# Optimization experiments

Measured on AMD Instinct MI355X. Metric: run time of the kernel, lower is better.

The kernel has to match this reference:

```python
import jax, jax.numpy as jnp
import numpy as np

N_NODES = 100000
N_EDGES = 1600000
NFEAT = 512
NHID = 64
NCLASS = 40


def setup_inputs() -> dict:
    key = jax.random.key(0)
    ks = jax.random.split(key, 8)
    x = jax.random.normal(ks[0], (N_NODES, NFEAT), dtype=jnp.float32)
    edge_row = jax.random.randint(ks[1], (N_EDGES,), 0, N_NODES, dtype=jnp.int32)
    edge_col = jax.random.randint(ks[2], (N_EDGES,), 0, N_NODES, dtype=jnp.int32)
    # normalized adjacency values (positive, small, like D^-1/2 A D^-1/2 entries)
    adj_vals = jax.random.uniform(ks[3], (N_EDGES,), dtype=jnp.float32) * 0.1
    # Glorot-style init as in Kipf's GraphConvolution reset_parameters
    W1 = jax.random.uniform(ks[4], (NFEAT, NHID), dtype=jnp.float32,
                            minval=-1.0, maxval=1.0) / jnp.sqrt(jnp.float32(NHID))
    b1 = jax.random.uniform(ks[5], (NHID,), dtype=jnp.float32,
                            minval=-1.0, maxval=1.0) / jnp.sqrt(jnp.float32(NHID))
    W10 = jax.random.uniform(ks[6], (NHID, NCLASS), dtype=jnp.float32,
                             minval=-1.0, maxval=1.0) / jnp.sqrt(jnp.float32(NCLASS))
    b10 = jax.random.uniform(ks[7], (NCLASS,), dtype=jnp.float32,
                             minval=-1.0, maxval=1.0) / jnp.sqrt(jnp.float32(NCLASS))
    return {"x": x, "adj_vals": adj_vals, "W1": W1, "b1": b1,
            "W10": W10, "b10": b10,
            "edge_row": edge_row, "edge_col": edge_col}


def reference(x, adj_vals, W1, b1, W10, b10, edge_row, edge_col):
    def spmm(vals, feat):
        # sparse adj (COO) @ dense feat: gather source rows, scale, scatter-add to dest
        msgs = vals[:, None] * feat[edge_col]          # [E, d]
        return jax.ops.segment_sum(msgs, edge_row, num_segments=N_NODES)

    # gc1: support = x @ W1; out = spmm(adj, support) + b1
    h = spmm(adj_vals, x @ W1) + b1                    # [N, NHID]
    h = jax.nn.relu(h)
    # dropout: eval mode -> identity
    # gc10
    out = spmm(adj_vals, h @ W10) + b10                # [N, NCLASS]
    return jax.nn.log_softmax(out, axis=1)
```

## Files before the change

### kernel.cpp

```cpp
#include <hip/hip_runtime.h>

#define NND 100000
#define NE  1600000
#define NF  512
#define NH  64
#define NC  40

#define BROWS 256
#define NB ((NND + BROWS - 1) / BROWS)
#define BCAP 4864
#define EPB 4096
#define NEB ((NE + EPB - 1) / EPB)
#define W10PAD 52
#define HPAD 68

typedef unsigned short u16;
typedef unsigned int   u32;
typedef __attribute__((ext_vector_type(8))) __bf16 bf16x8;
typedef __attribute__((ext_vector_type(8))) u16    u16x8;
typedef __attribute__((ext_vector_type(4))) float  f32x4;

__device__ __forceinline__ u16 f2bf(float f) {
  u32 u = __builtin_bit_cast(u32, f);
  u += 0x7FFFu + ((u >> 16) & 1u);
  return (u16)(u >> 16);
}
__device__ __forceinline__ u32 pack2(float a, float b) {
  return (u32)f2bf(a) | ((u32)f2bf(b) << 16);
}
__device__ __forceinline__ float bf2f(u16 h) {
  return __builtin_bit_cast(float, (u32)h << 16);
}
__device__ __forceinline__ bf16x8 pack8(const float4& a, const float4& b) {
  uint4 v;
  v.x = pack2(a.x, a.y); v.y = pack2(a.z, a.w);
  v.z = pack2(b.x, b.y); v.w = pack2(b.z, b.w);
  return __builtin_bit_cast(bf16x8, v);
}

__global__ __launch_bounds__(256) void w1t_k(const float* __restrict__ W1,
                                             u16* __restrict__ w1t,
                                             int* __restrict__ gcursor) {
  if (blockIdx.x == 0) {
    for (int i = threadIdx.x; i < NB; i += 256) gcursor[i] = 0;
  }
  int i = blockIdx.x * 256 + threadIdx.x;
  if (i >= NF * NH) return;
  int n = i >> 9, k = i & 511;
  w1t[i] = f2bf(W1[(size_t)k * NH + n]);
}

__global__ __launch_bounds__(256) void gemm1_k(const float* __restrict__ x,
                                               const u16* __restrict__ w1t,
                                               u16* __restrict__ out) {
  __shared__ u16 Bs[2][64][72];
  const int t = threadIdx.x, w = t >> 6, lane = t & 63;
  const int l15 = lane & 15, l4 = lane >> 4;
  const int rowBase = blockIdx.x * 128;
  const int r0 = rowBase + w * 32 + l15;
  const float* pa0 = x + (size_t)min(r0, NND - 1) * NF + l4 * 8;
  const float* pa1 = x + (size_t)min(r0 + 16, NND - 1) * NF + l4 * 8;

  f32x4 acc[2][4];
#pragma unroll
  for (int i = 0; i < 2; ++i)
#pragma unroll
    for (int j = 0; j < 4; ++j) acc[i][j] = (f32x4){0.f, 0.f, 0.f, 0.f};

  uint4  bR[2];
  float4 aR[2][2][2];

  auto issueB = [&](int k0) {
#pragma unroll
    for (int i = 0; i < 2; ++i) {
      int c = t + i * 256;
      bR[i] = *(const uint4*)(w1t + (size_t)(c >> 3) * NF + k0 + (c & 7) * 8);
    }
  };
  auto issueA = [&](int k0) {
#pragma unroll
    for (int s = 0; s < 2; ++s) {
      const float* q0 = pa0 + k0 + s * 32;
      const float* q1 = pa1 + k0 + s * 32;
      aR[0][s][0] = *(const float4*)(q0);
      aR[0][s][1] = *(const float4*)(q0 + 4);
      aR[1][s][0] = *(const float4*)(q1);
      aR[1][s][1] = *(const float4*)(q1 + 4);
    }
  };

  issueB(0);
  issueA(0);
  for (int it = 0; it < 8; ++it) {
    const int b = it & 1;
#pragma unroll
    for (int i = 0; i < 2; ++i) {
      int c = t + i * 256;
      *(uint4*)&Bs[b][c >> 3][(c & 7) * 8] = bR[i];
    }
    bf16x8 fa0[2], fa1[2];
#pragma unroll
    for (int s = 0; s < 2; ++s) {
      fa0[s] = pack8(aR[0][s][0], aR[0][s][1]);
      fa1[s] = pack8(aR[1][s][0], aR[1][s][1]);
    }
    if (it < 7) { issueB((it + 1) * 64); issueA((it + 1) * 64); }
    __syncthreads();
#pragma unroll
    for (int s = 0; s < 2; ++s) {
#pragma unroll
      for (int ct = 0; ct < 4; ++ct) {
        bf16x8 bb = *(const bf16x8*)&Bs[b][ct * 16 + l15][s * 32 + l4 * 8];
        acc[0][ct] = __builtin_amdgcn_mfma_f32_16x16x32_bf16(fa0[s], bb, acc[0][ct], 0, 0, 0);
        acc[1][ct] = __builtin_amdgcn_mfma_f32_16x16x32_bf16(fa1[s], bb, acc[1][ct], 0, 0, 0);
      }
    }
  }

#pragma unroll
  for (int rt = 0; rt < 2; ++rt)
#pragma unroll
    for (int ct = 0; ct < 4; ++ct)
#pragma unroll
      for (int i = 0; i < 4; ++i) {
        int row = rowBase + w * 32 + rt * 16 + l4 * 4 + i;
        if (row < NND) out[(size_t)row * NH + ct * 16 + l15] = f2bf(acc[rt][ct][i]);
      }
}

__global__ __launch_bounds__(1024) void bscatter_k(const float* __restrict__ vals,
                                                   const int* __restrict__ rows,
                                                   const int* __restrict__ cols,
                                                   int* __restrict__ gcursor,
                                                   int2* __restrict__ eb1) {
  __shared__ int cnt[NB];
  __shared__ int base[NB];
  const int t = threadIdx.x;
  for (int i = t; i < NB; i += 1024) cnt[i] = 0;
  __syncthreads();
  const int gb = blockIdx.x * EPB;
  int bin[4], rnk[4], rr[4], cc[4];
  float vv[4];
#pragma unroll
  for (int k = 0; k < 4; ++k) {
    int i = gb + t + k * 1024;
    if (i < NE) {
      rr[k] = rows[i]; cc[k] = cols[i]; vv[k] = vals[i];
      bin[k] = rr[k] >> 8;
      rnk[k] = atomicAdd(&cnt[bin[k]], 1);
    } else bin[k] = -1;
  }
  __syncthreads();
  for (int i = t; i < NB; i += 1024)
    if (cnt[i]) base[i] = i * BCAP + atomicAdd(&gcursor[i], cnt[i]);
  __syncthreads();
#pragma unroll
  for (int k = 0; k < 4; ++k) {
    if (bin[k] >= 0) {
      int pos = base[bin[k]] + rnk[k];
      eb1[pos] = make_int2((int)(((u32)cc[k] << 8) | (u32)(rr[k] & 255)),
                           __float_as_int(vv[k]));
    }
  }
}

__global__ __launch_bounds__(1024) void spmm1f_k(const int* __restrict__ gcursor,
                                                 const int2* __restrict__ eb1,
                                                 const u16* __restrict__ s1,
                                                 const float* __restrict__ b1,
                                                 const float* __restrict__ W10,
                                                 u16* __restrict__ s2) {
  __shared__ int2 se[BCAP];
  __shared__ u16 w10s[64 * W10PAD];
  __shared__ int cnt[BROWS];
  __shared__ int sc[BROWS];
  __shared__ int wsum[4];
  const int bkt = blockIdx.x, t = threadIdx.x;
  const int w = t >> 6, lane = t & 63;
  const int nE = min(gcursor[bkt], BCAP);
  const int beg = bkt * BCAP;
  for (int i = t; i < 64 * W10PAD; i += 1024) {
    int k = i / W10PAD, c = i - k * W10PAD;
    w10s[i] = (c < NC) ? f2bf(W10[k * NC + c]) : (u16)0;
  }
  if (t < BROWS) cnt[t] = 0;
  __syncthreads();
  int2 mye[5]; int myrow[5], myrank[5];
#pragma unroll
  for (int k = 0; k < 5; ++k) {
    int i = t + k * 1024;
    myrow[k] = -1;
    if (i < nE) {
      int2 e = eb1[beg + i];
      mye[k] = e;
      myrow[k] = e.x & 255;
      myrank[k] = atomicAdd(&cnt[myrow[k]], 1);
    }
  }
  __syncthreads();
  int c0 = 0, inc = 0;
  if (t < BROWS) {
    c0 = cnt[t]; inc = c0;
#pragma unroll
    for (int off = 1; off < 64; off <<= 1) {
      int u = __shfl_up(inc, off, 64);
      if ((t & 63) >= off) inc += u;
    }
    if ((t & 63) == 63) wsum[t >> 6] = inc;
  }
  __syncthreads();
  if (t < BROWS) {
    int pre = 0;
#pragma unroll
    for (int k = 0; k < 4; ++k) pre += (k < (t >> 6)) ? wsum[k] : 0;
    sc[t] = pre + inc - c0;
  }
  __syncthreads();
#pragma unroll
  for (int k = 0; k < 5; ++k)
    if (myrow[k] >= 0)
      se[sc[myrow[k]] + myrank[k]] = make_int2((int)((u32)mye[k].x >> 8), mye[k].y);
  __syncthreads();

  const float bias = b1[lane];
  float hreg[16];
#pragma unroll 1
  for (int i = 0; i < 16; ++i) {
    int r8 = w * 16 + i;
    int s = sc[r8], n = cnt[r8];
    float a0 = 0.f, a1 = 0.f, a2 = 0.f, a3 = 0.f;
    int j = 0;
    for (; j + 3 < n; j += 4) {
      int2 e0 = se[s + j], e1 = se[s + j + 1], e2 = se[s + j + 2], e3 = se[s + j + 3];
      a0 = fmaf(__int_as_float(e0.y), bf2f(s1[(size_t)e0.x * NH + lane]), a0);
      a1 = fmaf(__int_as_float(e1.y), bf2f(s1[(size_t)e1.x * NH + lane]), a1);
      a2 = fmaf(__int_as_float(e2.y), bf2f(s1[(size_t)e2.x * NH + lane]), a2);
      a3 = fmaf(__int_as_float(e3.y), bf2f(s1[(size_t)e3.x * NH + lane]), a3);
    }
    for (; j < n; ++j) {
      int2 e0 = se[s + j];
      a0 = fmaf(__int_as_float(e0.y), bf2f(s1[(size_t)e0.x * NH + lane]), a0);
    }
    hreg[i] = fmaxf((a0 + a1) + (a2 + a3) + bias, 0.f);
  }
  __syncthreads();

  u16* hl = (u16*)se + (size_t)w * 16 * HPAD;
#pragma unroll
  for (int i = 0; i < 16; ++i) hl[i * HPAD + lane] = f2bf(hreg[i]);

  const int l15 = lane & 15, l4 = lane >> 4;
  bf16x8 afr[2];
  afr[0] = *(const bf16x8*)&hl[l15 * HPAD + l4 * 8];
  afr[1] = *(const bf16x8*)&hl[l15 * HPAD + 32 + l4 * 8];

  f32x4 acc[3];
#pragma unroll
  for (int ct = 0; ct < 3; ++ct) acc[ct] = (f32x4){0.f, 0.f, 0.f, 0.f};
#pragma unroll
  for (int ct = 0; ct < 3; ++ct) {
#pragma unroll
    for (int kk = 0; kk < 2; ++kk) {
      u16x8 bw;
#pragma unroll
      for (int j = 0; j < 8; ++j)
        bw[j] = w10s[(kk * 32 + l4 * 8 + j) * W10PAD + ct * 16 + l15];
      acc[ct] = __builtin_amdgcn_mfma_f32_16x16x32_bf16(
          afr[kk], __builtin_bit_cast(bf16x8, bw), acc[ct], 0, 0, 0);
    }
  }
#pragma unroll
  for (int ct = 0; ct < 3; ++ct) {
    int c = ct * 16 + l15;
#pragma unroll
    for (int i = 0; i < 4; ++i) {
      int grow = bkt * BROWS + w * 16 + l4 * 4 + i;
      if (c < NC && grow < NND) s2[(size_t)grow * NC + c] = f2bf(acc[ct][i]);
    }
  }
}

__global__ __launch_bounds__(1024) void spmm2s_k(const int* __restrict__ gcursor,
                                                 const int2* __restrict__ eb1,
                                                 const u16* __restrict__ s2,
                                                 const float* __restrict__ b10,
                                                 float* __restrict__ out) {
  __shared__ int2 se[BCAP];
  __shared__ int cnt[BROWS];
  __shared__ int sc[BROWS];
  __shared__ int wsum[4];
  const int bkt = blockIdx.x, t = threadIdx.x;
  const int w = t >> 6, lane = t & 63;
  const int nE = min(gcursor[bkt], BCAP);
  const int beg = bkt * BCAP;
  if (t < BROWS) cnt[t] = 0;
  __syncthreads();
  int2 mye[5]; int myrow[5], myrank[5];
#pragma unroll
  for (int k = 0; k < 5; ++k) {
    int i = t + k * 1024;
    myrow[k] = -1;
    if (i < nE) {
      int2 e = eb1[beg + i];
      mye[k] = e;
      myrow[k] = e.x & 255;
      myrank[k] = atomicAdd(&cnt[myrow[k]], 1);
    }
  }
  __syncthreads();
  int c0 = 0, inc = 0;
  if (t < BROWS) {
    c0 = cnt[t]; inc = c0;
#pragma unroll
    for (int off = 1; off < 64; off <<= 1) {
      int u = __shfl_up(inc, off, 64);
      if ((t & 63) >= off) inc += u;
    }
    if ((t & 63) == 63) wsum[t >> 6] = inc;
  }
  __syncthreads();
  if (t < BROWS) {
    int pre = 0;
#pragma unroll
    for (int k = 0; k < 4; ++k) pre += (k < (t >> 6)) ? wsum[k] : 0;
    sc[t] = pre + inc - c0;
  }
  __syncthreads();
#pragma unroll
  for (int k = 0; k < 5; ++k)
    if (myrow[k] >= 0)
      se[sc[myrow[k]] + myrank[k]] = make_int2((int)((u32)mye[k].x >> 8), mye[k].y);
  __syncthreads();

  const int off0 = (lane < NC) ? lane : 0;
  const float bias = (lane < NC) ? b10[lane] : 0.f;
#pragma unroll 1
  for (int i = 0; i < 16; ++i) {
    int r8 = w * 16 + i;
    int s = sc[r8], n = cnt[r8];
    float a0 = 0.f, a1 = 0.f, a2 = 0.f, a3 = 0.f;
    int j = 0;
    for (; j + 3 < n; j += 4) {
      int2 e0 = se[s + j], e1 = se[s + j + 1], e2 = se[s + j + 2], e3 = se[s + j + 3];
      a0 = fmaf(__int_as_float(e0.y), bf2f(s2[(size_t)e0.x * NC + off0]), a0);
      a1 = fmaf(__int_as_float(e1.y), bf2f(s2[(size_t)e1.x * NC + off0]), a1);
      a2 = fmaf(__int_as_float(e2.y), bf2f(s2[(size_t)e2.x * NC + off0]), a2);
      a3 = fmaf(__int_as_float(e3.y), bf2f(s2[(size_t)e3.x * NC + off0]), a3);
    }
    for (; j < n; ++j) {
      int2 e0 = se[s + j];
      a0 = fmaf(__int_as_float(e0.y), bf2f(s2[(size_t)e0.x * NC + off0]), a0);
    }
    int grow = bkt * BROWS + r8;
    if (grow >= NND) continue;
    float vv = (lane < NC) ? (a0 + a1) + (a2 + a3) + bias : -INFINITY;
    float m = vv;
#pragma unroll
    for (int o = 32; o; o >>= 1) m = fmaxf(m, __shfl_xor(m, o, 64));
    float e = (lane < NC) ? __expf(vv - m) : 0.f;
    float ss = e;
#pragma unroll
    for (int o = 32; o; o >>= 1) ss += __shfl_xor(ss, o, 64);
    if (lane < NC) out[(size_t)grow * NC + lane] = vv - m - __logf(ss);
  }
}

extern "C" void kernel_launch(void* const* d_in, const int* in_sizes, int n_in,
                              void* d_out, int out_size, void* d_ws, size_t ws_size,
                              hipStream_t stream) {
  const float* x    = (const float*)d_in[0];
  const float* adj  = (const float*)d_in[1];
  const float* W1   = (const float*)d_in[2];
  const float* b1   = (const float*)d_in[3];
  const float* W10  = (const float*)d_in[4];
  const float* b10  = (const float*)d_in[5];
  const int*   erow = (const int*)d_in[6];
  const int*   ecol = (const int*)d_in[7];
  float* out = (float*)d_out;

  char* p = (char*)d_ws;
  u16*  s1  = (u16*)p;    p += (size_t)NND * NH * 2;
  u16*  s2  = (u16*)p;    p += (size_t)NND * NC * 2;
  u16*  w1t = (u16*)p;    p += (size_t)NF * NH * 2;
  int2* eb1 = (int2*)p;   p += (size_t)NB * BCAP * 8;
  int* gcursor = (int*)p;

  w1t_k<<<(NF * NH + 255) / 256, 256, 0, stream>>>(W1, w1t, gcursor);
  bscatter_k<<<NEB, 1024, 0, stream>>>(adj, erow, ecol, gcursor, eb1);

  gemm1_k<<<(NND + 127) / 128, 256, 0, stream>>>(x, w1t, s1);
  spmm1f_k<<<NB, 1024, 0, stream>>>(gcursor, eb1, s1, b1, W10, s2);
  spmm2s_k<<<NB, 1024, 0, stream>>>(gcursor, eb1, s2, b10, out);
}
```

Baseline: 199.4 us.

## Persist row-sorted bucket edges from spmm1 for reuse in spmm2; widen scatter blocks

The first SpMM kernel now writes its per-bucket, row-sorted edge list and per-row counts to workspace. The second SpMM kernel loads these directly instead of redoing the LDS atomic counting sort. This drops the atomics and one barrier from spmm2, at the cost of extra global writes in spmm1 and a second edge buffer. The scatter kernel also handles 8192 edges per block instead of 4096, which halves the number of blocks and cuts the global cursor atomics.

```diff
diff --git a/kernel.cpp b/kernel.cpp
--- a/kernel.cpp
+++ b/kernel.cpp
@@ -9,7 +9,7 @@
 #define BROWS 256
 #define NB ((NND + BROWS - 1) / BROWS)
 #define BCAP 4864
-#define EPB 4096
+#define EPB 8192
 #define NEB ((NE + EPB - 1) / EPB)
 #define W10PAD 52
 #define HPAD 68
@@ -139,10 +139,10 @@
   for (int i = t; i < NB; i += 1024) cnt[i] = 0;
   __syncthreads();
   const int gb = blockIdx.x * EPB;
-  int bin[4], rnk[4], rr[4], cc[4];
-  float vv[4];
-#pragma unroll
-  for (int k = 0; k < 4; ++k) {
+  int bin[8], rnk[8], rr[8], cc[8];
+  float vv[8];
+#pragma unroll
+  for (int k = 0; k < 8; ++k) {
     int i = gb + t + k * 1024;
     if (i < NE) {
       rr[k] = rows[i]; cc[k] = cols[i]; vv[k] = vals[i];
@@ -155,7 +155,7 @@
     if (cnt[i]) base[i] = i * BCAP + atomicAdd(&gcursor[i], cnt[i]);
   __syncthreads();
 #pragma unroll
-  for (int k = 0; k < 4; ++k) {
+  for (int k = 0; k < 8; ++k) {
     if (bin[k] >= 0) {
       int pos = base[bin[k]] + rnk[k];
       eb1[pos] = make_int2((int)(((u32)cc[k] << 8) | (u32)(rr[k] & 255)),
@@ -169,7 +169,9 @@
                                                  const u16* __restrict__ s1,
                                                  const float* __restrict__ b1,
                                                  const float* __restrict__ W10,
-                                                 u16* __restrict__ s2) {
+                                                 u16* __restrict__ s2,
+                                                 int2* __restrict__ eb2,
+                                                 int* __restrict__ rowcnt) {
   __shared__ int2 se[BCAP];
   __shared__ u16 w10s[64 * W10PAD];
   __shared__ int cnt[BROWS];
@@ -214,6 +216,7 @@
 #pragma unroll
     for (int k = 0; k < 4; ++k) pre += (k < (t >> 6)) ? wsum[k] : 0;
     sc[t] = pre + inc - c0;
+    rowcnt[bkt * BROWS + t] = c0;
   }
   __syncthreads();
 #pragma unroll
@@ -221,6 +224,12 @@
     if (myrow[k] >= 0)
       se[sc[myrow[k]] + myrank[k]] = make_int2((int)((u32)mye[k].x >> 8), mye[k].y);
   __syncthreads();
+
+#pragma unroll
+  for (int k = 0; k < 5; ++k) {
+    int i = t + k * 1024;
+    if (i < nE) eb2[beg + i] = se[i];
+  }
 
   const float bias = b1[lane];
   float hreg[16];
@@ -281,7 +290,8 @@
 }
 
 __global__ __launch_bounds__(1024) void spmm2s_k(const int* __restrict__ gcursor,
-                                                 const int2* __restrict__ eb1,
+                                                 const int2* __restrict__ eb2,
+                                                 const int* __restrict__ rowcnt,
                                                  const u16* __restrict__ s2,
                                                  const float* __restrict__ b10,
                                                  float* __restrict__ out) {
@@ -293,19 +303,11 @@
   const int w = t >> 6, lane = t & 63;
   const int nE = min(gcursor[bkt], BCAP);
   const int beg = bkt * BCAP;
-  if (t < BROWS) cnt[t] = 0;
-  __syncthreads();
-  int2 mye[5]; int myrow[5], myrank[5];
+  if (t < BROWS) cnt[t] = rowcnt[bkt * BROWS + t];
 #pragma unroll
   for (int k = 0; k < 5; ++k) {
     int i = t + k * 1024;
-    myrow[k] = -1;
-    if (i < nE) {
-      int2 e = eb1[beg + i];
-      mye[k] = e;
-      myrow[k] = e.x & 255;
-      myrank[k] = atomicAdd(&cnt[myrow[k]], 1);
-    }
+    if (i < nE) se[i] = eb2[beg + i];
   }
   __syncthreads();
   int c0 = 0, inc = 0;
@@ -325,11 +327,6 @@
     for (int k = 0; k < 4; ++k) pre += (k < (t >> 6)) ? wsum[k] : 0;
     sc[t] = pre + inc - c0;
   }
-  __syncthreads();
-#pragma unroll
-  for (int k = 0; k < 5; ++k)
-    if (myrow[k] >= 0)
-      se[sc[myrow[k]] + myrank[k]] = make_int2((int)((u32)mye[k].x >> 8), mye[k].y);
   __syncthreads();
 
   const int off0 = (lane < NC) ? lane : 0;
@@ -383,12 +380,14 @@
   u16*  s2  = (u16*)p;    p += (size_t)NND * NC * 2;
   u16*  w1t = (u16*)p;    p += (size_t)NF * NH * 2;
   int2* eb1 = (int2*)p;   p += (size_t)NB * BCAP * 8;
+  int2* eb2 = (int2*)p;   p += (size_t)NB * BCAP * 8;
+  int* rowcnt = (int*)p;  p += (size_t)NB * BROWS * 4;
   int* gcursor = (int*)p;
 
   w1t_k<<<(NF * NH + 255) / 256, 256, 0, stream>>>(W1, w1t, gcursor);
   bscatter_k<<<NEB, 1024, 0, stream>>>(adj, erow, ecol, gcursor, eb1);
 
   gemm1_k<<<(NND + 127) / 128, 256, 0, stream>>>(x, w1t, s1);
-  spmm1f_k<<<NB, 1024, 0, stream>>>(gcursor, eb1, s1, b1, W10, s2);
-  spmm2s_k<<<NB, 1024, 0, stream>>>(gcursor, eb1, s2, b10, out);
-}
+  spmm1f_k<<<NB, 1024, 0, stream>>>(gcursor, eb1, s1, b1, W10, s2, eb2, rowcnt);
+  spmm2s_k<<<NB, 1024, 0, stream>>>(gcursor, eb2, rowcnt, s2, b10, out);
+}
```

Result: no change. 198.7 us (-0.3%).
